# Kernel optimization log

Hardware: AMD Instinct MI355X
Metric: run time of the kernel (lower is better)

Reference implementation:

```python
import jax, jax.numpy as jnp
import numpy as np

REG_STD = jnp.asarray([0.1, 0.1, 0.2, 0.2, 0.1], dtype=jnp.float32)  # normalize() target_std, mean=0


def setup_inputs() -> dict:
    key = jax.random.key(0)
    ks = jax.random.split(key, 8)
    B, N, C, R = 2, 2048, 256, 7
    D, H, NCLS = C * R * R, 1024, 10
    features = jax.random.normal(ks[0], (B, N, C, R, R), jnp.float32)
    boxes = jax.random.uniform(ks[1], (B, N, 5), jnp.float32)  # cx,cy,w,h,angle (stride units)
    strides = jnp.ones((B, N, 5), jnp.float32)
    W1 = jax.random.normal(ks[2], (D, H), jnp.float32) * 0.02
    b1 = jnp.zeros((H,), jnp.float32)
    W2 = jax.random.normal(ks[3], (H, H), jnp.float32) * 0.02
    b2 = jnp.zeros((H,), jnp.float32)
    Wc = jax.random.normal(ks[4], (H, NCLS + 1), jnp.float32) * 0.02
    bc = jnp.zeros((NCLS + 1,), jnp.float32)
    Wr = jax.random.normal(ks[5], (H, 5), jnp.float32) * 0.02
    br = jnp.zeros((5,), jnp.float32)
    return {"features": features, "boxes": boxes, "strides": strides,
            "W1": W1, "b1": b1, "W2": W2, "b2": b2,
            "Wc": Wc, "bc": bc, "Wr": Wr, "br": br}


def reference(features, boxes, strides, W1, b1, W2, b2, Wc, bc, Wr, br):
    B, N = features.shape[:2]
    x = features.reshape(B, N, -1)                      # [B,N,C*7*7] (Flatten start_dim=2)
    h = jax.nn.relu(jnp.einsum('bnd,dh->bnh', x, W1) + b1)
    h = jax.nn.relu(jnp.einsum('bnh,hk->bnk', h, W2) + b2)
    classification = jnp.einsum('bnh,hc->bnc', h, Wc) + bc   # [B,N,num_classes+1]
    regression = (jnp.einsum('bnh,hr->bnr', h, Wr) + br) * REG_STD  # normalize: mean 0, std per-channel
    # rois: proposal boxes scaled back to image coords (all but angle)
    rois = boxes.at[..., :4].multiply(strides[..., :4])
    # box decode (delta-style for x,y; exp for w,h,angle)
    bx = boxes[..., 2] * regression[..., 0] + boxes[..., 0]
    by = boxes[..., 3] * regression[..., 1] + boxes[..., 1]
    bw = boxes[..., 2] * jnp.exp(regression[..., 2])
    bh = boxes[..., 3] * jnp.exp(regression[..., 3])
    ba = boxes[..., 4] * jnp.exp(regression[..., 4])
    dec = jnp.stack((bx, by, bw, bh, ba), axis=-1)
    dec = dec.at[..., :4].multiply(strides[..., :4])
    return classification, dec, rois
```

## Files before the change

kernel.cpp:

```cpp
#include <hip/hip_runtime.h>
#include <hip/hip_bf16.h>
#include <stdint.h>

typedef unsigned short u16;
typedef unsigned int u32;
typedef float f32x4 __attribute__((ext_vector_type(4)));
typedef short bf16x8 __attribute__((ext_vector_type(8)));

#define DEV static __device__ __forceinline__

DEV u16 f2bf(float x) {
    u32 u = __float_as_uint(x);
    u32 r = (u + 0x7fffu + ((u >> 16) & 1u)) >> 16;
    return (u16)r;
}
DEV float bf2f(u16 u) { return __uint_as_float(((u32)u) << 16); }
DEV u32 pk2bf(float lo, float hi) {
    u32 r;
    asm("v_cvt_pk_bf16_f32 %0, %1, %2" : "=v"(r) : "v"(lo), "v"(hi));
    return r;
}


__global__ __launch_bounds__(256) void k_transpose_cvt(const float* __restrict__ in,
                                                       u16* __restrict__ out,
                                                       int K, int N) {
    __shared__ float tile[32][33];
    int tiles_n = N >> 5;
    int tk = blockIdx.x / tiles_n, tn = blockIdx.x % tiles_n;
    int tx = threadIdx.x & 31, ty = threadIdx.x >> 5;
    int k0 = tk * 32, n0 = tn * 32;
#pragma unroll
    for (int i = 0; i < 4; ++i)
        tile[ty * 4 + i][tx] = in[(size_t)(k0 + ty * 4 + i) * N + n0 + tx];
    __syncthreads();
#pragma unroll
    for (int i = 0; i < 4; ++i)
        out[(size_t)(n0 + ty * 4 + i) * K + k0 + tx] = f2bf(tile[tx][ty * 4 + i]);
}

__global__ __launch_bounds__(256) void k_pack_head(const float* __restrict__ Wc,
                                                   const float* __restrict__ Wr,
                                                   float* __restrict__ Whead) {
    int r = blockIdx.x * 256 + threadIdx.x;
    if (r >= 1024) return;
    float* o = Whead + (size_t)r * 16;
#pragma unroll
    for (int c = 0; c < 11; ++c) o[c] = Wc[(size_t)r * 11 + c];
#pragma unroll
    for (int c = 0; c < 5; ++c) o[11 + c] = Wr[(size_t)r * 5 + c];
}

__global__ __launch_bounds__(256, 4) void k_gemm1(
    const float* __restrict__ A, const u16* __restrict__ Bt,
    float* __restrict__ P, int M, int N, int K, int KHALF) {
    __shared__ u16 As[128 * 64];
    __shared__ u16 Bs[64 * 64];

    int nwg = gridDim.x;
    int cpx = nwg >> 3;
    int bid = blockIdx.x;
    int swz = (bid & 7) * cpx + (bid >> 3);
    int split = swz >> 9;
    int tile = swz & 511;
    int bm = tile >> 4, bn = tile & 15;

    int tid = threadIdx.x;
    int lane = tid & 63, wid = tid >> 6;
    int wm = wid >> 1, wn = wid & 1;
    const int tm0 = bm * 128, tn0 = bn * 64;
    const int kbeg = split * KHALF;

    const int l8 = lane >> 3, l7 = lane & 7;
    const int bsrc = ((l7 ^ l8) << 3);

    f32x4 acc[4][2] = {};

    int kt = KHALF >> 6;
    for (int t = 0; t < kt; ++t) {
        int k0 = kbeg + (t << 6);
#pragma unroll
        for (int i = 0; i < 2; ++i) {
            int seg = wid * 2 + i;
            const u16* g = Bt + (size_t)(tn0 + seg * 8 + l8) * K + k0 + bsrc;
            __builtin_amdgcn_global_load_lds(
                (const __attribute__((address_space(1))) u32*)g,
                (__attribute__((address_space(3))) u32*)&Bs[seg * 512], 16, 0, 0);
        }
#pragma unroll
        for (int h = 0; h < 2; ++h) {
            float4 fa[2][2];
#pragma unroll
            for (int i = 0; i < 2; ++i) {
                int s = (h * 2 + i) * 256 + tid;
                int r = s >> 3, cg = s & 7;
                const float* g = A + (size_t)(tm0 + r) * K + k0 + cg * 8;
                fa[i][0] = *(const float4*)g;
                fa[i][1] = *(const float4*)(g + 4);
            }
#pragma unroll
            for (int i = 0; i < 2; ++i) {
                int s = (h * 2 + i) * 256 + tid;
                int r = s >> 3, cg = s & 7;
                u32 pk[4];
                pk[0] = pk2bf(fa[i][0].x, fa[i][0].y);
                pk[1] = pk2bf(fa[i][0].z, fa[i][0].w);
                pk[2] = pk2bf(fa[i][1].x, fa[i][1].y);
                pk[3] = pk2bf(fa[i][1].z, fa[i][1].w);
                int cb = (cg << 4) ^ ((r & 7) << 4);
                *(uint4*)((char*)As + r * 128 + cb) = *(const uint4*)pk;
            }
        }
        __syncthreads();

#pragma unroll
        for (int kk = 0; kk < 2; ++kk) {
            int cb = (kk << 6) + ((lane >> 4) << 4);
            bf16x8 a[4], b[2];
#pragma unroll
            for (int m = 0; m < 4; ++m) {
                int r = wm * 64 + m * 16 + (lane & 15);
                a[m] = *(const bf16x8*)((const char*)As + r * 128 + (cb ^ ((r & 7) << 4)));
            }
#pragma unroll
            for (int n = 0; n < 2; ++n) {
                int r = wn * 32 + n * 16 + (lane & 15);
                b[n] = *(const bf16x8*)((const char*)Bs + r * 128 + (cb ^ ((r & 7) << 4)));
            }
#pragma unroll
            for (int m = 0; m < 4; ++m)
#pragma unroll
                for (int n = 0; n < 2; ++n)
                    acc[m][n] = __builtin_amdgcn_mfma_f32_16x16x32_bf16(
                        a[m], b[n], acc[m][n], 0, 0, 0);
        }
        __syncthreads();
    }

    float* Ps = P + (size_t)split * M * N;
    int cr = lane >> 4, cc = lane & 15;
#pragma unroll
    for (int n = 0; n < 2; ++n) {
        int col = tn0 + wn * 32 + n * 16 + cc;
#pragma unroll
        for (int m = 0; m < 4; ++m) {
            int row0 = tm0 + wm * 64 + m * 16 + cr * 4;
#pragma unroll
            for (int r = 0; r < 4; ++r)
                Ps[(size_t)(row0 + r) * N + col] = acc[m][n][r];
        }
    }
}

__global__ __launch_bounds__(256) void k_combine(const float* __restrict__ P,
                                                 const float* __restrict__ bias,
                                                 u16* __restrict__ out,
                                                 int MN, int N) {
    int i = blockIdx.x * 256 + threadIdx.x;
    int ncol8 = N >> 3;
    int row = i / ncol8, c8 = i - row * ncol8;
    size_t off = (size_t)row * N + (size_t)c8 * 8;
    const float4* p0 = (const float4*)(P + off);
    const float4* p1 = (const float4*)(P + (size_t)MN + off);
    const float4* bp = (const float4*)(bias + (size_t)c8 * 8);
    float4 a0 = p0[0], a1 = p0[1];
    float4 b0 = p1[0], b1 = p1[1];
    float4 q0 = bp[0], q1 = bp[1];
    float v0 = fmaxf(a0.x + b0.x + q0.x, 0.f), v1 = fmaxf(a0.y + b0.y + q0.y, 0.f);
    float v2 = fmaxf(a0.z + b0.z + q0.z, 0.f), v3 = fmaxf(a0.w + b0.w + q0.w, 0.f);
    float v4 = fmaxf(a1.x + b1.x + q1.x, 0.f), v5 = fmaxf(a1.y + b1.y + q1.y, 0.f);
    float v6 = fmaxf(a1.z + b1.z + q1.z, 0.f), v7 = fmaxf(a1.w + b1.w + q1.w, 0.f);
    u32 pk[4] = {pk2bf(v0, v1), pk2bf(v2, v3), pk2bf(v4, v5), pk2bf(v6, v7)};
    *(uint4*)(out + off) = *(const uint4*)pk;
}

__global__ __launch_bounds__(256) void k_gemm2(
    const u16* __restrict__ A, const u16* __restrict__ Bt,
    const float* __restrict__ bias, u16* __restrict__ C,
    int M, int N, int K) {
    __shared__ u16 As[128 * 64];
    __shared__ u16 Bs[64 * 64];

    int nwg = gridDim.x;
    int cpx = nwg >> 3;
    int bid = blockIdx.x;
    int swz = (bid & 7) * cpx + (bid >> 3);
    int ntn = N >> 6;
    int bm = swz / ntn, bn = swz % ntn;

    int tid = threadIdx.x;
    int lane = tid & 63, wid = tid >> 6;
    int wm = wid >> 1, wn = wid & 1;
    const int tm0 = bm * 128, tn0 = bn * 64;

    const int l8 = lane >> 3, l7 = lane & 7;
    const int bsrc = ((l7 ^ l8) << 3);

    f32x4 acc[4][2] = {};

    int kt = K >> 6;
    for (int t = 0; t < kt; ++t) {
        int k0 = t << 6;
#pragma unroll
        for (int i = 0; i < 4; ++i) {
            int seg = wid * 4 + i;
            const u16* g = A + (size_t)(tm0 + seg * 8 + l8) * K + k0 + bsrc;
            __builtin_amdgcn_global_load_lds(
                (const __attribute__((address_space(1))) u32*)g,
                (__attribute__((address_space(3))) u32*)&As[seg * 512], 16, 0, 0);
        }
#pragma unroll
        for (int i = 0; i < 2; ++i) {
            int seg = wid * 2 + i;
            const u16* g = Bt + (size_t)(tn0 + seg * 8 + l8) * K + k0 + bsrc;
            __builtin_amdgcn_global_load_lds(
                (const __attribute__((address_space(1))) u32*)g,
                (__attribute__((address_space(3))) u32*)&Bs[seg * 512], 16, 0, 0);
        }
        __syncthreads();

#pragma unroll
        for (int kk = 0; kk < 2; ++kk) {
            int cb = (kk << 6) + ((lane >> 4) << 4);
            bf16x8 a[4], b[2];
#pragma unroll
            for (int m = 0; m < 4; ++m) {
                int r = wm * 64 + m * 16 + (lane & 15);
                a[m] = *(const bf16x8*)((const char*)As + r * 128 + (cb ^ ((r & 7) << 4)));
            }
#pragma unroll
            for (int n = 0; n < 2; ++n) {
                int r = wn * 32 + n * 16 + (lane & 15);
                b[n] = *(const bf16x8*)((const char*)Bs + r * 128 + (cb ^ ((r & 7) << 4)));
            }
#pragma unroll
            for (int m = 0; m < 4; ++m)
#pragma unroll
                for (int n = 0; n < 2; ++n)
                    acc[m][n] = __builtin_amdgcn_mfma_f32_16x16x32_bf16(
                        a[m], b[n], acc[m][n], 0, 0, 0);
        }
        __syncthreads();
    }

    int cr = lane >> 4, cc = lane & 15;
#pragma unroll
    for (int n = 0; n < 2; ++n) {
        int col = tn0 + wn * 32 + n * 16 + cc;
        float bv = bias[col];
#pragma unroll
        for (int m = 0; m < 4; ++m) {
            int row0 = tm0 + wm * 64 + m * 16 + cr * 4;
#pragma unroll
            for (int r = 0; r < 4; ++r) {
                float v = fmaxf(acc[m][n][r] + bv, 0.0f);
                C[(size_t)(row0 + r) * N + col] = f2bf(v);
            }
        }
    }
}

__global__ __launch_bounds__(256) void k_head(
    const u16* __restrict__ h2, const float* __restrict__ Whead,
    const float* __restrict__ bc, const float* __restrict__ br,
    const float* __restrict__ boxes, const float* __restrict__ strides,
    float* __restrict__ cls_out, float* __restrict__ dec_out,
    float* __restrict__ rois_out) {
    int lane = threadIdx.x & 63;
    int row = blockIdx.x * 4 + (threadIdx.x >> 6);

    const u16* hr = h2 + (size_t)row * 1024;
    float acc[16];
#pragma unroll
    for (int i = 0; i < 16; ++i) acc[i] = 0.0f;

#pragma unroll
    for (int j = 0; j < 16; ++j) {
        int k = j * 64 + lane;
        float h = bf2f(hr[k]);
        const float4* wp = (const float4*)(Whead + (size_t)k * 16);
        float4 q0 = wp[0], q1 = wp[1], q2 = wp[2], q3 = wp[3];
        acc[0]  = fmaf(h, q0.x, acc[0]);  acc[1]  = fmaf(h, q0.y, acc[1]);
        acc[2]  = fmaf(h, q0.z, acc[2]);  acc[3]  = fmaf(h, q0.w, acc[3]);
        acc[4]  = fmaf(h, q1.x, acc[4]);  acc[5]  = fmaf(h, q1.y, acc[5]);
        acc[6]  = fmaf(h, q1.z, acc[6]);  acc[7]  = fmaf(h, q1.w, acc[7]);
        acc[8]  = fmaf(h, q2.x, acc[8]);  acc[9]  = fmaf(h, q2.y, acc[9]);
        acc[10] = fmaf(h, q2.z, acc[10]); acc[11] = fmaf(h, q2.w, acc[11]);
        acc[12] = fmaf(h, q3.x, acc[12]); acc[13] = fmaf(h, q3.y, acc[13]);
        acc[14] = fmaf(h, q3.z, acc[14]); acc[15] = fmaf(h, q3.w, acc[15]);
    }
#pragma unroll
    for (int i = 0; i < 16; ++i) {
#pragma unroll
        for (int off = 32; off > 0; off >>= 1)
            acc[i] += __shfl_xor(acc[i], off);
    }

    if (lane == 0) {
        float* co = cls_out + (size_t)row * 11;
#pragma unroll
        for (int c = 0; c < 11; ++c) co[c] = acc[c] + bc[c];

        const float STD[5] = {0.1f, 0.1f, 0.2f, 0.2f, 0.1f};
        float reg[5];
#pragma unroll
        for (int j = 0; j < 5; ++j) reg[j] = (acc[11 + j] + br[j]) * STD[j];

        const float* bx = boxes + (size_t)row * 5;
        const float* st = strides + (size_t)row * 5;
        float b0 = bx[0], b1 = bx[1], b2 = bx[2], b3 = bx[3], b4 = bx[4];
        float s0 = st[0], s1 = st[1], s2 = st[2], s3 = st[3];

        float dx = b2 * reg[0] + b0;
        float dy = b3 * reg[1] + b1;
        float dw = b2 * expf(reg[2]);
        float dh = b3 * expf(reg[3]);
        float da = b4 * expf(reg[4]);

        float* dd = dec_out + (size_t)row * 5;
        dd[0] = dx * s0; dd[1] = dy * s1; dd[2] = dw * s2; dd[3] = dh * s3; dd[4] = da;

        float* rr = rois_out + (size_t)row * 5;
        rr[0] = b0 * s0; rr[1] = b1 * s1; rr[2] = b2 * s2; rr[3] = b3 * s3; rr[4] = b4;
    }
}

extern "C" void kernel_launch(void* const* d_in, const int* in_sizes, int n_in,
                              void* d_out, int out_size, void* d_ws, size_t ws_size,
                              hipStream_t stream) {
    const float* features = (const float*)d_in[0];
    const float* boxes    = (const float*)d_in[1];
    const float* strides  = (const float*)d_in[2];
    const float* W1 = (const float*)d_in[3];
    const float* b1 = (const float*)d_in[4];
    const float* W2 = (const float*)d_in[5];
    const float* b2 = (const float*)d_in[6];
    const float* Wc = (const float*)d_in[7];
    const float* bc = (const float*)d_in[8];
    const float* Wr = (const float*)d_in[9];
    const float* br = (const float*)d_in[10];

    const int M = 4096;
    const int K = 12544;
    const int H = 1024;

    char* ws = (char*)d_ws;
    u16*   W1T   = (u16*)(ws + 0);
    u16*   W2T   = (u16*)(ws + 25690112);
    float* Whead = (float*)(ws + 27787264);
    float* P     = (float*)(ws + 27852800);
    u16*   h1    = (u16*)(ws + 61407232);
    u16*   h2    = (u16*)(ws + 69795840);

    k_transpose_cvt<<<(K / 32) * (H / 32), 256, 0, stream>>>(W1, W1T, K, H);
    k_transpose_cvt<<<(H / 32) * (H / 32), 256, 0, stream>>>(W2, W2T, H, H);
    k_pack_head<<<4, 256, 0, stream>>>(Wc, Wr, Whead);

    k_gemm1<<<1024, 256, 0, stream>>>(features, W1T, P, M, H, K, K / 2);
    k_combine<<<(M * H / 8) / 256, 256, 0, stream>>>(P, b1, h1, M * H, H);
    k_gemm2<<<(M / 128) * (H / 64), 256, 0, stream>>>(h1, W2T, b2, h2, M, H, H);

    float* cls  = (float*)d_out;
    float* dec  = cls + (size_t)4096 * 11;
    float* rois = dec + (size_t)4096 * 5;
    k_head<<<1024, 256, 0, stream>>>(h2, Whead, bc, br, boxes, strides, cls, dec, rois);
}
```

Baseline: 616.2 us.

## Double-buffer LDS in both GEMMs and raise gemm1 split-K to four

Both GEMM kernels now use two LDS buffers so the next K-tile's global loads (register-staged fp32 A and direct-to-LDS B) are issued before the MFMA work on the current tile, removing one barrier-bound stall per iteration. The first-layer GEMM splits K four ways instead of two, doubling the grid, and the combine kernel sums four partial buffers. This trades more LDS per block (fewer resident blocks) and an extra fp32 partial-sum write/read for better latency hiding and more parallelism; workspace offsets are moved to fit the larger partial buffer.

```diff
diff --git a/kernel.cpp b/kernel.cpp
--- a/kernel.cpp
+++ b/kernel.cpp
@@ -51,68 +51,88 @@
     for (int c = 0; c < 5; ++c) o[11 + c] = Wr[(size_t)r * 5 + c];
 }
 
-__global__ __launch_bounds__(256, 4) void k_gemm1(
+__global__ __launch_bounds__(256, 3) void k_gemm1(
     const float* __restrict__ A, const u16* __restrict__ Bt,
-    float* __restrict__ P, int M, int N, int K, int KHALF) {
-    __shared__ u16 As[128 * 64];
-    __shared__ u16 Bs[64 * 64];
+    float* __restrict__ P, int M, int N, int K, int KS) {
+    __shared__ u16 As[2][128 * 64];
+    __shared__ u16 Bs[2][64 * 64];
 
     int nwg = gridDim.x;
     int cpx = nwg >> 3;
     int bid = blockIdx.x;
     int swz = (bid & 7) * cpx + (bid >> 3);
     int split = swz >> 9;
-    int tile = swz & 511;
-    int bm = tile >> 4, bn = tile & 15;
+    int rest = swz & 511;
+    int bm = rest >> 4, bn = rest & 15;
 
     int tid = threadIdx.x;
     int lane = tid & 63, wid = tid >> 6;
     int wm = wid >> 1, wn = wid & 1;
     const int tm0 = bm * 128, tn0 = bn * 64;
-    const int kbeg = split * KHALF;
+    const int kbeg = split * KS;
 
     const int l8 = lane >> 3, l7 = lane & 7;
     const int bsrc = ((l7 ^ l8) << 3);
 
-    f32x4 acc[4][2] = {};
-
-    int kt = KHALF >> 6;
-    for (int t = 0; t < kt; ++t) {
-        int k0 = kbeg + (t << 6);
+    int s0r[4], s0c[4];
+#pragma unroll
+    for (int i = 0; i < 4; ++i) {
+        int s = i * 256 + tid;
+        s0r[i] = s >> 3;
+        s0c[i] = s & 7;
+    }
+
+    auto loadA = [&](int k0, float4* fa) {
+#pragma unroll
+        for (int i = 0; i < 4; ++i) {
+            const float* g = A + (size_t)(tm0 + s0r[i]) * K + k0 + s0c[i] * 8;
+            fa[2 * i]     = *(const float4*)g;
+            fa[2 * i + 1] = *(const float4*)(g + 4);
+        }
+    };
+    auto writeA = [&](u16* as, const float4* fa) {
+#pragma unroll
+        for (int i = 0; i < 4; ++i) {
+            u32 pk[4];
+            pk[0] = pk2bf(fa[2 * i].x,     fa[2 * i].y);
+            pk[1] = pk2bf(fa[2 * i].z,     fa[2 * i].w);
+            pk[2] = pk2bf(fa[2 * i + 1].x, fa[2 * i + 1].y);
+            pk[3] = pk2bf(fa[2 * i + 1].z, fa[2 * i + 1].w);
+            int r = s0r[i];
+            *(uint4*)((char*)as + r * 128 + ((s0c[i] << 4) ^ ((r & 7) << 4))) =
+                *(const uint4*)pk;
+        }
+    };
+    auto stageB = [&](u16* bs, int k0) {
 #pragma unroll
         for (int i = 0; i < 2; ++i) {
             int seg = wid * 2 + i;
             const u16* g = Bt + (size_t)(tn0 + seg * 8 + l8) * K + k0 + bsrc;
             __builtin_amdgcn_global_load_lds(
                 (const __attribute__((address_space(1))) u32*)g,
-                (__attribute__((address_space(3))) u32*)&Bs[seg * 512], 16, 0, 0);
-        }
-#pragma unroll
-        for (int h = 0; h < 2; ++h) {
-            float4 fa[2][2];
-#pragma unroll
-            for (int i = 0; i < 2; ++i) {
-                int s = (h * 2 + i) * 256 + tid;
-                int r = s >> 3, cg = s & 7;
-                const float* g = A + (size_t)(tm0 + r) * K + k0 + cg * 8;
-                fa[i][0] = *(const float4*)g;
-                fa[i][1] = *(const float4*)(g + 4);
-            }
-#pragma unroll
-            for (int i = 0; i < 2; ++i) {
-                int s = (h * 2 + i) * 256 + tid;
-                int r = s >> 3, cg = s & 7;
-                u32 pk[4];
-                pk[0] = pk2bf(fa[i][0].x, fa[i][0].y);
-                pk[1] = pk2bf(fa[i][0].z, fa[i][0].w);
-                pk[2] = pk2bf(fa[i][1].x, fa[i][1].y);
-                pk[3] = pk2bf(fa[i][1].z, fa[i][1].w);
-                int cb = (cg << 4) ^ ((r & 7) << 4);
-                *(uint4*)((char*)As + r * 128 + cb) = *(const uint4*)pk;
-            }
-        }
-        __syncthreads();
-
+                (__attribute__((address_space(3))) u32*)(bs + seg * 512), 16, 0, 0);
+        }
+    };
+
+    f32x4 acc[4][2] = {};
+    float4 fa[8];
+
+    int kt = KS >> 6;
+    loadA(kbeg, fa);
+    stageB(Bs[0], kbeg);
+    writeA(As[0], fa);
+    __syncthreads();
+
+    int cur = 0;
+    for (int t = 0; t < kt; ++t) {
+        int k1 = kbeg + ((t + 1) << 6);
+        if (t + 1 < kt) {
+            loadA(k1, fa);
+            stageB(Bs[cur ^ 1], k1);
+        }
+
+        const u16* as = As[cur];
+        const u16* bs = Bs[cur];
 #pragma unroll
         for (int kk = 0; kk < 2; ++kk) {
             int cb = (kk << 6) + ((lane >> 4) << 4);
@@ -120,12 +140,12 @@
 #pragma unroll
             for (int m = 0; m < 4; ++m) {
                 int r = wm * 64 + m * 16 + (lane & 15);
-                a[m] = *(const bf16x8*)((const char*)As + r * 128 + (cb ^ ((r & 7) << 4)));
+                a[m] = *(const bf16x8*)((const char*)as + r * 128 + (cb ^ ((r & 7) << 4)));
             }
 #pragma unroll
             for (int n = 0; n < 2; ++n) {
                 int r = wn * 32 + n * 16 + (lane & 15);
-                b[n] = *(const bf16x8*)((const char*)Bs + r * 128 + (cb ^ ((r & 7) << 4)));
+                b[n] = *(const bf16x8*)((const char*)bs + r * 128 + (cb ^ ((r & 7) << 4)));
             }
 #pragma unroll
             for (int m = 0; m < 4; ++m)
@@ -134,7 +154,10 @@
                     acc[m][n] = __builtin_amdgcn_mfma_f32_16x16x32_bf16(
                         a[m], b[n], acc[m][n], 0, 0, 0);
         }
+
+        if (t + 1 < kt) writeA(As[cur ^ 1], fa);
         __syncthreads();
+        cur ^= 1;
     }
 
     float* Ps = P + (size_t)split * M * N;
@@ -160,26 +183,36 @@
     int ncol8 = N >> 3;
     int row = i / ncol8, c8 = i - row * ncol8;
     size_t off = (size_t)row * N + (size_t)c8 * 8;
-    const float4* p0 = (const float4*)(P + off);
-    const float4* p1 = (const float4*)(P + (size_t)MN + off);
+    float v[8];
+    {
+        const float4* p = (const float4*)(P + off);
+        float4 a = p[0], b = p[1];
+        v[0] = a.x; v[1] = a.y; v[2] = a.z; v[3] = a.w;
+        v[4] = b.x; v[5] = b.y; v[6] = b.z; v[7] = b.w;
+    }
+#pragma unroll
+    for (int s = 1; s < 4; ++s) {
+        const float4* p = (const float4*)(P + (size_t)s * MN + off);
+        float4 a = p[0], b = p[1];
+        v[0] += a.x; v[1] += a.y; v[2] += a.z; v[3] += a.w;
+        v[4] += b.x; v[5] += b.y; v[6] += b.z; v[7] += b.w;
+    }
     const float4* bp = (const float4*)(bias + (size_t)c8 * 8);
-    float4 a0 = p0[0], a1 = p0[1];
-    float4 b0 = p1[0], b1 = p1[1];
     float4 q0 = bp[0], q1 = bp[1];
-    float v0 = fmaxf(a0.x + b0.x + q0.x, 0.f), v1 = fmaxf(a0.y + b0.y + q0.y, 0.f);
-    float v2 = fmaxf(a0.z + b0.z + q0.z, 0.f), v3 = fmaxf(a0.w + b0.w + q0.w, 0.f);
-    float v4 = fmaxf(a1.x + b1.x + q1.x, 0.f), v5 = fmaxf(a1.y + b1.y + q1.y, 0.f);
-    float v6 = fmaxf(a1.z + b1.z + q1.z, 0.f), v7 = fmaxf(a1.w + b1.w + q1.w, 0.f);
-    u32 pk[4] = {pk2bf(v0, v1), pk2bf(v2, v3), pk2bf(v4, v5), pk2bf(v6, v7)};
+    float w0 = fmaxf(v[0] + q0.x, 0.f), w1 = fmaxf(v[1] + q0.y, 0.f);
+    float w2 = fmaxf(v[2] + q0.z, 0.f), w3 = fmaxf(v[3] + q0.w, 0.f);
+    float w4 = fmaxf(v[4] + q1.x, 0.f), w5 = fmaxf(v[5] + q1.y, 0.f);
+    float w6 = fmaxf(v[6] + q1.z, 0.f), w7 = fmaxf(v[7] + q1.w, 0.f);
+    u32 pk[4] = {pk2bf(w0, w1), pk2bf(w2, w3), pk2bf(w4, w5), pk2bf(w6, w7)};
     *(uint4*)(out + off) = *(const uint4*)pk;
 }
 
-__global__ __launch_bounds__(256) void k_gemm2(
+__global__ __launch_bounds__(256, 3) void k_gemm2(
     const u16* __restrict__ A, const u16* __restrict__ Bt,
     const float* __restrict__ bias, u16* __restrict__ C,
     int M, int N, int K) {
-    __shared__ u16 As[128 * 64];
-    __shared__ u16 Bs[64 * 64];
+    __shared__ u16 As[2][128 * 64];
+    __shared__ u16 Bs[2][64 * 64];
 
     int nwg = gridDim.x;
     int cpx = nwg >> 3;
@@ -196,18 +229,14 @@
     const int l8 = lane >> 3, l7 = lane & 7;
     const int bsrc = ((l7 ^ l8) << 3);
 
-    f32x4 acc[4][2] = {};
-
-    int kt = K >> 6;
-    for (int t = 0; t < kt; ++t) {
-        int k0 = t << 6;
+    auto stage = [&](u16* as, u16* bs, int k0) {
 #pragma unroll
         for (int i = 0; i < 4; ++i) {
             int seg = wid * 4 + i;
             const u16* g = A + (size_t)(tm0 + seg * 8 + l8) * K + k0 + bsrc;
             __builtin_amdgcn_global_load_lds(
                 (const __attribute__((address_space(1))) u32*)g,
-                (__attribute__((address_space(3))) u32*)&As[seg * 512], 16, 0, 0);
+                (__attribute__((address_space(3))) u32*)(as + seg * 512), 16, 0, 0);
         }
 #pragma unroll
         for (int i = 0; i < 2; ++i) {
@@ -215,10 +244,22 @@
             const u16* g = Bt + (size_t)(tn0 + seg * 8 + l8) * K + k0 + bsrc;
             __builtin_amdgcn_global_load_lds(
                 (const __attribute__((address_space(1))) u32*)g,
-                (__attribute__((address_space(3))) u32*)&Bs[seg * 512], 16, 0, 0);
-        }
-        __syncthreads();
-
+                (__attribute__((address_space(3))) u32*)(bs + seg * 512), 16, 0, 0);
+        }
+    };
+
+    f32x4 acc[4][2] = {};
+
+    int kt = K >> 6;
+    stage(As[0], Bs[0], 0);
+    __syncthreads();
+
+    int cur = 0;
+    for (int t = 0; t < kt; ++t) {
+        if (t + 1 < kt) stage(As[cur ^ 1], Bs[cur ^ 1], (t + 1) << 6);
+
+        const u16* as = As[cur];
+        const u16* bs = Bs[cur];
 #pragma unroll
         for (int kk = 0; kk < 2; ++kk) {
             int cb = (kk << 6) + ((lane >> 4) << 4);
@@ -226,12 +267,12 @@
 #pragma unroll
             for (int m = 0; m < 4; ++m) {
                 int r = wm * 64 + m * 16 + (lane & 15);
-                a[m] = *(const bf16x8*)((const char*)As + r * 128 + (cb ^ ((r & 7) << 4)));
+                a[m] = *(const bf16x8*)((const char*)as + r * 128 + (cb ^ ((r & 7) << 4)));
             }
 #pragma unroll
             for (int n = 0; n < 2; ++n) {
                 int r = wn * 32 + n * 16 + (lane & 15);
-                b[n] = *(const bf16x8*)((const char*)Bs + r * 128 + (cb ^ ((r & 7) << 4)));
+                b[n] = *(const bf16x8*)((const char*)bs + r * 128 + (cb ^ ((r & 7) << 4)));
             }
 #pragma unroll
             for (int m = 0; m < 4; ++m)
@@ -241,6 +282,7 @@
                         a[m], b[n], acc[m][n], 0, 0, 0);
         }
         __syncthreads();
+        cur ^= 1;
     }
 
     int cr = lane >> 4, cc = lane & 15;
@@ -349,14 +391,14 @@
     u16*   W2T   = (u16*)(ws + 25690112);
     float* Whead = (float*)(ws + 27787264);
     float* P     = (float*)(ws + 27852800);
-    u16*   h1    = (u16*)(ws + 61407232);
-    u16*   h2    = (u16*)(ws + 69795840);
+    u16*   h1    = (u16*)(ws + 94961664);
+    u16*   h2    = (u16*)(ws + 103350272);
 
     k_transpose_cvt<<<(K / 32) * (H / 32), 256, 0, stream>>>(W1, W1T, K, H);
     k_transpose_cvt<<<(H / 32) * (H / 32), 256, 0, stream>>>(W2, W2T, H, H);
     k_pack_head<<<4, 256, 0, stream>>>(Wc, Wr, Whead);
 
-    k_gemm1<<<1024, 256, 0, stream>>>(features, W1T, P, M, H, K, K / 2);
+    k_gemm1<<<2048, 256, 0, stream>>>(features, W1T, P, M, H, K, K / 4);
     k_combine<<<(M * H / 8) / 256, 256, 0, stream>>>(P, b1, h1, M * H, H);
     k_gemm2<<<(M / 128) * (H / 64), 256, 0, stream>>>(h1, W2T, b2, h2, M, H, H);
 
```

After: 587.0 us. 1.05x faster.

## Pre-convert features to bf16 and enlarge GEMM tiles to 128x128

Applied to the files above, without the earlier changes.

Adds a separate pass that converts the fp32 features to bf16 once, so GEMM1 can load both operands straight into LDS with global_load_lds instead of loading and converting fp32 A in every N-tile. Both GEMMs move from 128x64 to 128x128 tiles, halving how often A is re-read and giving each wave more MFMA work. The split-K partials are stored as fp16, halving that traffic, and h1/h2 reuse the partial buffer. The head kernel now reads Wc/Wr directly, dropping the packing kernel. The trade-offs are an extra full pass over the large feature tensor, fewer GEMM1 workgroups (512) for occupancy, and some precision loss from fp16 partials.

```diff
diff --git a/kernel.cpp b/kernel.cpp
--- a/kernel.cpp
+++ b/kernel.cpp
@@ -4,6 +4,7 @@
 
 typedef unsigned short u16;
 typedef unsigned int u32;
+typedef _Float16 f16;
 typedef float f32x4 __attribute__((ext_vector_type(4)));
 typedef short bf16x8 __attribute__((ext_vector_type(8)));
 
@@ -20,7 +21,19 @@
     asm("v_cvt_pk_bf16_f32 %0, %1, %2" : "=v"(r) : "v"(lo), "v"(hi));
     return r;
 }
-
+DEV u16 f2h(float x) { f16 v = (f16)x; return *(u16*)&v; }
+DEV float h2f(u16 u) { f16 v = *(f16*)&u; return (float)v; }
+
+
+__global__ __launch_bounds__(256) void k_cvt_bf16(const float* __restrict__ in,
+                                                  u16* __restrict__ out, int n8) {
+    int i = blockIdx.x * 256 + threadIdx.x;
+    if (i >= n8) return;
+    const float4* p = (const float4*)in + (size_t)i * 2;
+    float4 a = p[0], b = p[1];
+    u32 pk[4] = {pk2bf(a.x, a.y), pk2bf(a.z, a.w), pk2bf(b.x, b.y), pk2bf(b.z, b.w)};
+    *(uint4*)(out + (size_t)i * 8) = *(const uint4*)pk;
+}
 
 __global__ __launch_bounds__(256) void k_transpose_cvt(const float* __restrict__ in,
                                                        u16* __restrict__ out,
@@ -39,120 +52,92 @@
         out[(size_t)(n0 + ty * 4 + i) * K + k0 + tx] = f2bf(tile[tx][ty * 4 + i]);
 }
 
-__global__ __launch_bounds__(256) void k_pack_head(const float* __restrict__ Wc,
-                                                   const float* __restrict__ Wr,
-                                                   float* __restrict__ Whead) {
-    int r = blockIdx.x * 256 + threadIdx.x;
-    if (r >= 1024) return;
-    float* o = Whead + (size_t)r * 16;
-#pragma unroll
-    for (int c = 0; c < 11; ++c) o[c] = Wc[(size_t)r * 11 + c];
-#pragma unroll
-    for (int c = 0; c < 5; ++c) o[11 + c] = Wr[(size_t)r * 5 + c];
-}
-
-__global__ __launch_bounds__(256, 4) void k_gemm1(
-    const float* __restrict__ A, const u16* __restrict__ Bt,
-    float* __restrict__ P, int M, int N, int K, int KHALF) {
+__global__ __launch_bounds__(256) void k_gemm1(
+    const u16* __restrict__ A, const u16* __restrict__ Bt,
+    u16* __restrict__ P, int M, int N, int K, int KS) {
     __shared__ u16 As[128 * 64];
-    __shared__ u16 Bs[64 * 64];
+    __shared__ u16 Bs[128 * 64];
 
     int nwg = gridDim.x;
     int cpx = nwg >> 3;
     int bid = blockIdx.x;
     int swz = (bid & 7) * cpx + (bid >> 3);
-    int split = swz >> 9;
-    int tile = swz & 511;
-    int bm = tile >> 4, bn = tile & 15;
+    int split = swz >> 8;
+    int rest = swz & 255;
+    int bm = rest >> 3, bn = rest & 7;
 
     int tid = threadIdx.x;
     int lane = tid & 63, wid = tid >> 6;
     int wm = wid >> 1, wn = wid & 1;
-    const int tm0 = bm * 128, tn0 = bn * 64;
-    const int kbeg = split * KHALF;
+    const int tm0 = bm * 128, tn0 = bn * 128;
+    const int kbeg = split * KS;
 
     const int l8 = lane >> 3, l7 = lane & 7;
     const int bsrc = ((l7 ^ l8) << 3);
 
-    f32x4 acc[4][2] = {};
-
-    int kt = KHALF >> 6;
+    f32x4 acc[4][4] = {};
+
+    int kt = KS >> 6;
     for (int t = 0; t < kt; ++t) {
         int k0 = kbeg + (t << 6);
 #pragma unroll
-        for (int i = 0; i < 2; ++i) {
-            int seg = wid * 2 + i;
+        for (int i = 0; i < 4; ++i) {
+            int seg = wid * 4 + i;
+            const u16* g = A + (size_t)(tm0 + seg * 8 + l8) * K + k0 + bsrc;
+            __builtin_amdgcn_global_load_lds(
+                (const __attribute__((address_space(1))) u32*)g,
+                (__attribute__((address_space(3))) u32*)&As[seg * 512], 16, 0, 0);
+        }
+#pragma unroll
+        for (int i = 0; i < 4; ++i) {
+            int seg = wid * 4 + i;
             const u16* g = Bt + (size_t)(tn0 + seg * 8 + l8) * K + k0 + bsrc;
             __builtin_amdgcn_global_load_lds(
                 (const __attribute__((address_space(1))) u32*)g,
                 (__attribute__((address_space(3))) u32*)&Bs[seg * 512], 16, 0, 0);
         }
-#pragma unroll
-        for (int h = 0; h < 2; ++h) {
-            float4 fa[2][2];
-#pragma unroll
-            for (int i = 0; i < 2; ++i) {
-                int s = (h * 2 + i) * 256 + tid;
-                int r = s >> 3, cg = s & 7;
-                const float* g = A + (size_t)(tm0 + r) * K + k0 + cg * 8;
-                fa[i][0] = *(const float4*)g;
-                fa[i][1] = *(const float4*)(g + 4);
-            }
-#pragma unroll
-            for (int i = 0; i < 2; ++i) {
-                int s = (h * 2 + i) * 256 + tid;
-                int r = s >> 3, cg = s & 7;
-                u32 pk[4];
-                pk[0] = pk2bf(fa[i][0].x, fa[i][0].y);
-                pk[1] = pk2bf(fa[i][0].z, fa[i][0].w);
-                pk[2] = pk2bf(fa[i][1].x, fa[i][1].y);
-                pk[3] = pk2bf(fa[i][1].z, fa[i][1].w);
-                int cb = (cg << 4) ^ ((r & 7) << 4);
-                *(uint4*)((char*)As + r * 128 + cb) = *(const uint4*)pk;
-            }
-        }
         __syncthreads();
 
 #pragma unroll
         for (int kk = 0; kk < 2; ++kk) {
             int cb = (kk << 6) + ((lane >> 4) << 4);
-            bf16x8 a[4], b[2];
+            bf16x8 a[4], b[4];
 #pragma unroll
             for (int m = 0; m < 4; ++m) {
                 int r = wm * 64 + m * 16 + (lane & 15);
                 a[m] = *(const bf16x8*)((const char*)As + r * 128 + (cb ^ ((r & 7) << 4)));
             }
 #pragma unroll
-            for (int n = 0; n < 2; ++n) {
-                int r = wn * 32 + n * 16 + (lane & 15);
+            for (int n = 0; n < 4; ++n) {
+                int r = wn * 64 + n * 16 + (lane & 15);
                 b[n] = *(const bf16x8*)((const char*)Bs + r * 128 + (cb ^ ((r & 7) << 4)));
             }
 #pragma unroll
             for (int m = 0; m < 4; ++m)
 #pragma unroll
-                for (int n = 0; n < 2; ++n)
+                for (int n = 0; n < 4; ++n)
                     acc[m][n] = __builtin_amdgcn_mfma_f32_16x16x32_bf16(
                         a[m], b[n], acc[m][n], 0, 0, 0);
         }
         __syncthreads();
     }
 
-    float* Ps = P + (size_t)split * M * N;
+    u16* Ps = P + (size_t)split * M * N;
     int cr = lane >> 4, cc = lane & 15;
 #pragma unroll
-    for (int n = 0; n < 2; ++n) {
-        int col = tn0 + wn * 32 + n * 16 + cc;
+    for (int n = 0; n < 4; ++n) {
+        int col = tn0 + wn * 64 + n * 16 + cc;
 #pragma unroll
         for (int m = 0; m < 4; ++m) {
             int row0 = tm0 + wm * 64 + m * 16 + cr * 4;
 #pragma unroll
             for (int r = 0; r < 4; ++r)
-                Ps[(size_t)(row0 + r) * N + col] = acc[m][n][r];
-        }
-    }
-}
-
-__global__ __launch_bounds__(256) void k_combine(const float* __restrict__ P,
+                Ps[(size_t)(row0 + r) * N + col] = f2h(acc[m][n][r]);
+        }
+    }
+}
+
+__global__ __launch_bounds__(256) void k_combine(const u16* __restrict__ P,
                                                  const float* __restrict__ bias,
                                                  u16* __restrict__ out,
                                                  int MN, int N) {
@@ -160,17 +145,20 @@
     int ncol8 = N >> 3;
     int row = i / ncol8, c8 = i - row * ncol8;
     size_t off = (size_t)row * N + (size_t)c8 * 8;
-    const float4* p0 = (const float4*)(P + off);
-    const float4* p1 = (const float4*)(P + (size_t)MN + off);
+    uint4 r0 = *(const uint4*)(P + off);
+    uint4 r1 = *(const uint4*)(P + (size_t)MN + off);
+    const u16* a = (const u16*)&r0;
+    const u16* b = (const u16*)&r1;
     const float4* bp = (const float4*)(bias + (size_t)c8 * 8);
-    float4 a0 = p0[0], a1 = p0[1];
-    float4 b0 = p1[0], b1 = p1[1];
     float4 q0 = bp[0], q1 = bp[1];
-    float v0 = fmaxf(a0.x + b0.x + q0.x, 0.f), v1 = fmaxf(a0.y + b0.y + q0.y, 0.f);
-    float v2 = fmaxf(a0.z + b0.z + q0.z, 0.f), v3 = fmaxf(a0.w + b0.w + q0.w, 0.f);
-    float v4 = fmaxf(a1.x + b1.x + q1.x, 0.f), v5 = fmaxf(a1.y + b1.y + q1.y, 0.f);
-    float v6 = fmaxf(a1.z + b1.z + q1.z, 0.f), v7 = fmaxf(a1.w + b1.w + q1.w, 0.f);
-    u32 pk[4] = {pk2bf(v0, v1), pk2bf(v2, v3), pk2bf(v4, v5), pk2bf(v6, v7)};
+    float v[8];
+#pragma unroll
+    for (int j = 0; j < 8; ++j) v[j] = h2f(a[j]) + h2f(b[j]);
+    v[0] = fmaxf(v[0] + q0.x, 0.f); v[1] = fmaxf(v[1] + q0.y, 0.f);
+    v[2] = fmaxf(v[2] + q0.z, 0.f); v[3] = fmaxf(v[3] + q0.w, 0.f);
+    v[4] = fmaxf(v[4] + q1.x, 0.f); v[5] = fmaxf(v[5] + q1.y, 0.f);
+    v[6] = fmaxf(v[6] + q1.z, 0.f); v[7] = fmaxf(v[7] + q1.w, 0.f);
+    u32 pk[4] = {pk2bf(v[0], v[1]), pk2bf(v[2], v[3]), pk2bf(v[4], v[5]), pk2bf(v[6], v[7])};
     *(uint4*)(out + off) = *(const uint4*)pk;
 }
 
@@ -179,24 +167,24 @@
     const float* __restrict__ bias, u16* __restrict__ C,
     int M, int N, int K) {
     __shared__ u16 As[128 * 64];
-    __shared__ u16 Bs[64 * 64];
+    __shared__ u16 Bs[128 * 64];
 
     int nwg = gridDim.x;
     int cpx = nwg >> 3;
     int bid = blockIdx.x;
     int swz = (bid & 7) * cpx + (bid >> 3);
-    int ntn = N >> 6;
+    int ntn = N >> 7;
     int bm = swz / ntn, bn = swz % ntn;
 
     int tid = threadIdx.x;
     int lane = tid & 63, wid = tid >> 6;
     int wm = wid >> 1, wn = wid & 1;
-    const int tm0 = bm * 128, tn0 = bn * 64;
+    const int tm0 = bm * 128, tn0 = bn * 128;
 
     const int l8 = lane >> 3, l7 = lane & 7;
     const int bsrc = ((l7 ^ l8) << 3);
 
-    f32x4 acc[4][2] = {};
+    f32x4 acc[4][4] = {};
 
     int kt = K >> 6;
     for (int t = 0; t < kt; ++t) {
@@ -210,8 +198,8 @@
                 (__attribute__((address_space(3))) u32*)&As[seg * 512], 16, 0, 0);
         }
 #pragma unroll
-        for (int i = 0; i < 2; ++i) {
-            int seg = wid * 2 + i;
+        for (int i = 0; i < 4; ++i) {
+            int seg = wid * 4 + i;
             const u16* g = Bt + (size_t)(tn0 + seg * 8 + l8) * K + k0 + bsrc;
             __builtin_amdgcn_global_load_lds(
                 (const __attribute__((address_space(1))) u32*)g,
@@ -222,21 +210,21 @@
 #pragma unroll
         for (int kk = 0; kk < 2; ++kk) {
             int cb = (kk << 6) + ((lane >> 4) << 4);
-            bf16x8 a[4], b[2];
+            bf16x8 a[4], b[4];
 #pragma unroll
             for (int m = 0; m < 4; ++m) {
                 int r = wm * 64 + m * 16 + (lane & 15);
                 a[m] = *(const bf16x8*)((const char*)As + r * 128 + (cb ^ ((r & 7) << 4)));
             }
 #pragma unroll
-            for (int n = 0; n < 2; ++n) {
-                int r = wn * 32 + n * 16 + (lane & 15);
+            for (int n = 0; n < 4; ++n) {
+                int r = wn * 64 + n * 16 + (lane & 15);
                 b[n] = *(const bf16x8*)((const char*)Bs + r * 128 + (cb ^ ((r & 7) << 4)));
             }
 #pragma unroll
             for (int m = 0; m < 4; ++m)
 #pragma unroll
-                for (int n = 0; n < 2; ++n)
+                for (int n = 0; n < 4; ++n)
                     acc[m][n] = __builtin_amdgcn_mfma_f32_16x16x32_bf16(
                         a[m], b[n], acc[m][n], 0, 0, 0);
         }
@@ -245,8 +233,8 @@
 
     int cr = lane >> 4, cc = lane & 15;
 #pragma unroll
-    for (int n = 0; n < 2; ++n) {
-        int col = tn0 + wn * 32 + n * 16 + cc;
+    for (int n = 0; n < 4; ++n) {
+        int col = tn0 + wn * 64 + n * 16 + cc;
         float bv = bias[col];
 #pragma unroll
         for (int m = 0; m < 4; ++m) {
@@ -261,7 +249,8 @@
 }
 
 __global__ __launch_bounds__(256) void k_head(
-    const u16* __restrict__ h2, const float* __restrict__ Whead,
+    const u16* __restrict__ h2, const float* __restrict__ Wc,
+    const float* __restrict__ Wr,
     const float* __restrict__ bc, const float* __restrict__ br,
     const float* __restrict__ boxes, const float* __restrict__ strides,
     float* __restrict__ cls_out, float* __restrict__ dec_out,
@@ -278,16 +267,12 @@
     for (int j = 0; j < 16; ++j) {
         int k = j * 64 + lane;
         float h = bf2f(hr[k]);
-        const float4* wp = (const float4*)(Whead + (size_t)k * 16);
-        float4 q0 = wp[0], q1 = wp[1], q2 = wp[2], q3 = wp[3];
-        acc[0]  = fmaf(h, q0.x, acc[0]);  acc[1]  = fmaf(h, q0.y, acc[1]);
-        acc[2]  = fmaf(h, q0.z, acc[2]);  acc[3]  = fmaf(h, q0.w, acc[3]);
-        acc[4]  = fmaf(h, q1.x, acc[4]);  acc[5]  = fmaf(h, q1.y, acc[5]);
-        acc[6]  = fmaf(h, q1.z, acc[6]);  acc[7]  = fmaf(h, q1.w, acc[7]);
-        acc[8]  = fmaf(h, q2.x, acc[8]);  acc[9]  = fmaf(h, q2.y, acc[9]);
-        acc[10] = fmaf(h, q2.z, acc[10]); acc[11] = fmaf(h, q2.w, acc[11]);
-        acc[12] = fmaf(h, q3.x, acc[12]); acc[13] = fmaf(h, q3.y, acc[13]);
-        acc[14] = fmaf(h, q3.z, acc[14]); acc[15] = fmaf(h, q3.w, acc[15]);
+        const float* wc = Wc + (size_t)k * 11;
+        const float* wr = Wr + (size_t)k * 5;
+#pragma unroll
+        for (int c = 0; c < 11; ++c) acc[c] = fmaf(h, wc[c], acc[c]);
+#pragma unroll
+        for (int c = 0; c < 5; ++c) acc[11 + c] = fmaf(h, wr[c], acc[11 + c]);
     }
 #pragma unroll
     for (int i = 0; i < 16; ++i) {
@@ -345,23 +330,23 @@
     const int H = 1024;
 
     char* ws = (char*)d_ws;
-    u16*   W1T   = (u16*)(ws + 0);
-    u16*   W2T   = (u16*)(ws + 25690112);
-    float* Whead = (float*)(ws + 27787264);
-    float* P     = (float*)(ws + 27852800);
-    u16*   h1    = (u16*)(ws + 61407232);
-    u16*   h2    = (u16*)(ws + 69795840);
-
+    u16* Abf = (u16*)(ws + 0);
+    u16* W1T = (u16*)(ws + 102760448);
+    u16* W2T = (u16*)(ws + 128450560);
+    u16* P   = (u16*)(ws + 130547712);
+    u16* h1  = P;
+    u16* h2  = P + (size_t)M * H;
+
+    k_cvt_bf16<<<25088, 256, 0, stream>>>(features, Abf, 6422528);
     k_transpose_cvt<<<(K / 32) * (H / 32), 256, 0, stream>>>(W1, W1T, K, H);
     k_transpose_cvt<<<(H / 32) * (H / 32), 256, 0, stream>>>(W2, W2T, H, H);
-    k_pack_head<<<4, 256, 0, stream>>>(Wc, Wr, Whead);
-
-    k_gemm1<<<1024, 256, 0, stream>>>(features, W1T, P, M, H, K, K / 2);
+
+    k_gemm1<<<512, 256, 0, stream>>>(Abf, W1T, P, M, H, K, K / 2);
     k_combine<<<(M * H / 8) / 256, 256, 0, stream>>>(P, b1, h1, M * H, H);
-    k_gemm2<<<(M / 128) * (H / 64), 256, 0, stream>>>(h1, W2T, b2, h2, M, H, H);
+    k_gemm2<<<(M / 128) * (H / 128), 256, 0, stream>>>(h1, W2T, b2, h2, M, H, H);
 
     float* cls  = (float*)d_out;
     float* dec  = cls + (size_t)4096 * 11;
     float* rois = dec + (size_t)4096 * 5;
-    k_head<<<1024, 256, 0, stream>>>(h2, Whead, bc, br, boxes, strides, cls, dec, rois);
-}
+    k_head<<<1024, 256, 0, stream>>>(h2, Wc, Wr, bc, br, boxes, strides, cls, dec, rois);
+}
```

Measured after the change: 534.3 us. 13.3% less time.
